# Kernel tuning notes

Measured on AMD Instinct MI355X. Metric: run time of the kernel, lower is better.

Reference implementation:

```python
import jax, jax.numpy as jnp
import numpy as np

B, F, V, K, D, H = 16384, 26, 100000, 16, 13, 400
IN_DIM = F * K + D  # 429
EPS = 1e-5


def _bn(x, g, b):
    # BatchNorm1d in training mode: batch statistics (biased var, like torch)
    m = jnp.mean(x, axis=0)
    v = jnp.mean((x - m) ** 2, axis=0)
    return g * (x - m) / jnp.sqrt(v + EPS) + b


def setup_inputs() -> dict:
    key = jax.random.key(0)
    ks = jax.random.split(key, 12)
    X_cat = jax.random.randint(ks[0], (B, F), 0, V)
    X_dense = jax.random.normal(ks[1], (B, D), dtype=jnp.float32)
    fm1_tables = jax.random.normal(ks[2], (F, V, 1), dtype=jnp.float32) * 0.01
    emb_tables = jax.random.normal(ks[3], (F, V, K), dtype=jnp.float32) * 0.01
    Wd = jax.random.normal(ks[4], (D, 1), dtype=jnp.float32) * 0.1
    bd = jnp.zeros((1,), jnp.float32)
    W1 = jax.random.normal(ks[5], (IN_DIM, H), dtype=jnp.float32) * (1.0 / np.sqrt(IN_DIM))
    b1 = jnp.zeros((H,), jnp.float32)
    g1 = jnp.ones((H,), jnp.float32)
    be1 = jnp.zeros((H,), jnp.float32)
    W2 = jax.random.normal(ks[6], (H, H), dtype=jnp.float32) * (1.0 / np.sqrt(H))
    b2 = jnp.zeros((H,), jnp.float32)
    g2 = jnp.ones((H,), jnp.float32)
    be2 = jnp.zeros((H,), jnp.float32)
    W3 = jax.random.normal(ks[7], (H, 1), dtype=jnp.float32) * (1.0 / np.sqrt(H))
    b3 = jnp.zeros((1,), jnp.float32)
    return dict(X_cat=X_cat, X_dense=X_dense, fm1_tables=fm1_tables,
                emb_tables=emb_tables, Wd=Wd, bd=bd, W1=W1, b1=b1, g1=g1,
                be1=be1, W2=W2, b2=b2, g2=g2, be2=be2, W3=W3, b3=b3)


def reference(X_cat, X_dense, fm1_tables, emb_tables, Wd, bd,
              W1, b1, g1, be1, W2, b2, g2, be2, W3, b3):
    gather = jax.vmap(lambda tab, idx: tab[idx], in_axes=(0, 1), out_axes=1)
    # 1st order: [B, F, 1] -> sum over fields -> [B, 1]
    y_1st = jnp.sum(gather(fm1_tables, X_cat), axis=1) + X_dense @ Wd + bd
    # 2nd order embeddings: [B, F, K]
    emb = gather(emb_tables, X_cat)
    s = jnp.sum(emb, axis=1)                 # [B, K]
    ix = s ** 2 - jnp.sum(emb ** 2, axis=1)  # [B, K]
    fm_y = 0.5 * jnp.sum(ix, axis=1, keepdims=True)
    # DNN on [flattened embeddings, dense]
    x = jnp.concatenate([emb.reshape(emb.shape[0], -1), X_dense], axis=1)
    h = jax.nn.relu(_bn(x @ W1 + b1, g1, be1))
    h = jax.nn.relu(_bn(h @ W2 + b2, g2, be2))
    dnn_y = h @ W3 + b3
    return y_1st + fm_y + dnn_y
```

## Files before the change

### kernel.cpp

```cpp
#include <hip/hip_runtime.h>
#include <stdint.h>

#define B_ROWS 16384
#define NF 26
#define NV 100000
#define ND 13
#define NH 400
#define XPAD 448
#define ZPAD 416
#define EPS 1e-5f

typedef __attribute__((ext_vector_type(8))) short short8;
typedef __attribute__((ext_vector_type(4))) float f32x4;
typedef __attribute__((ext_vector_type(4))) unsigned int uint4v;

__device__ inline float bf2f(unsigned short u) {
    union { unsigned int i; float f; } v; v.i = (unsigned int)u << 16; return v.f;
}
__device__ inline unsigned short f2bf(float f) {
    union { float f; unsigned int i; } v; v.f = f;
    return (unsigned short)((v.i + 0x7fff + ((v.i >> 16) & 1)) >> 16);
}

typedef __attribute__((address_space(1))) const unsigned int g_u32;
typedef __attribute__((address_space(3))) unsigned int l_u32;
__device__ __forceinline__ void gload_lds16(const void* g, void* l) {
    __builtin_amdgcn_global_load_lds((g_u32*)g, (l_u32*)l, 16, 0, 0);
}

#define X_OFF    0
#define Z1_OFF   14680064
#define W1S_OFF  28311552
#define W2S_OFF  28712960
#define BASE_OFF 29085696
#define ST_OFF   29151232

__global__ __launch_bounds__(256) void gather_prep(
    const int* __restrict__ Xcat, const float* __restrict__ Xdense,
    const float* __restrict__ fm1, const float* __restrict__ emb,
    const float* __restrict__ Wd, const float* __restrict__ bd,
    const float* __restrict__ W1, const float* __restrict__ W2,
    unsigned short* __restrict__ X, float* __restrict__ base,
    unsigned short* __restrict__ W1s, unsigned short* __restrict__ W2s,
    float* __restrict__ st)
{
    int tid = threadIdx.x;
    if (blockIdx.x >= 1024) {
        int c = (blockIdx.x - 1024) * 256 + tid;
        if (c < 256) {
            for (int i = tid; i < 6656; i += 256) st[i] = 0.f;
        }
        const float* W; unsigned short* dst; int K; int cc;
        if (c < 25088) { W = W1; dst = W1s; K = 429; cc = c; }
        else           { W = W2; dst = W2s; K = 400; cc = c - 25088; }
        int n  = cc % 448;
        int q  = (cc / 448) & 3;
        int kt = cc / 1792;
        unsigned short o[8];
        #pragma unroll
        for (int j = 0; j < 8; ++j) {
            int k = kt * 32 + q * 8 + j;
            float v = (n < NH && k < K) ? W[(size_t)k * NH + n] : 0.f;
            o[j] = f2bf(v);
        }
        *(uint4v*)(dst + (size_t)cc * 8) = *(uint4v*)o;
        return;
    }
    int r = blockIdx.x * 16 + (tid >> 4);
    int k = tid & 15;
    const int* idxp = Xcat + (size_t)r * NF;
    unsigned short* xrow = X + (size_t)r * XPAD;

    float s = 0.f, ss = 0.f;
    #pragma unroll
    for (int f = 0; f < NF; ++f) {
        int idx = idxp[f];
        float v = emb[((size_t)f * NV + idx) * 16 + k];
        s += v; ss += v * v;
        xrow[f * 16 + k] = f2bf(v);
    }
    float fmsum = fm1[(size_t)k * NV + idxp[k]];
    if (k < NF - 16) fmsum += fm1[(size_t)(k + 16) * NV + idxp[k + 16]];
    float dsum = 0.f;
    if (k < ND) {
        float xd = Xdense[(size_t)r * ND + k];
        dsum = xd * Wd[k];
        xrow[NF * 16 + k] = f2bf(xd);
    }
    xrow[429 + k] = 0;
    if (k < 3) xrow[445 + k] = 0;

    float ix = s * s - ss;
    float rf = fmsum, rd = dsum;
    #pragma unroll
    for (int off = 8; off; off >>= 1) {
        ix += __shfl_xor(ix, off, 16);
        rf += __shfl_xor(rf, off, 16);
        rd += __shfl_xor(rd, off, 16);
    }
    if (k == 0) base[r] = 0.5f * ix + rf + rd + bd[0];
}

template<int NT, int LDA, bool APPLY_BN>
__global__ __launch_bounds__(512, 2) void gemm_v2(
    const unsigned short* __restrict__ A,
    const unsigned short* __restrict__ Wst,
    const float* __restrict__ bias,
    const float* __restrict__ st_all,
    const float* __restrict__ g, const float* __restrict__ be,
    unsigned short* __restrict__ Z, int ldz, int padZ,
    float* __restrict__ st_out, int sumOff, int sqOff)
{
    __shared__ __align__(16) unsigned short slices[25600];
    __shared__ float alpha_s[416], beta_s[416];

    const int tid = threadIdx.x, bid = blockIdx.x;
    const int lane = tid & 63, wv = tid >> 6;
    const int rg = wv >> 2, w4 = wv & 3;
    const int l15 = lane & 15, qh = lane >> 4;
    const int cb = (w4 == 0) ? 0 : (112 + (w4 - 1) * 96);
    const int NFW = (w4 == 0) ? 7 : 6;
    unsigned short* slice =
        slices + rg * 12800 + ((w4 == 0) ? 0 : (3584 + (w4 - 1) * 3072));
    const int arowA = bid * 64 + rg * 32 + l15;
    const int arowB = arowA + 16;

    if constexpr (APPLY_BN) {
        for (int c = tid; c < ZPAD; c += 512) {
            float a = 0.f, b = 0.f;
            if (c < NH) {
                float gs = 0.f, gq = 0.f;
                #pragma unroll
                for (int cp = 0; cp < 4; ++cp) {
                    gs += st_all[cp * 1664 + c];
                    gq += st_all[cp * 1664 + 416 + c];
                }
                float mean = gs * (1.f / 16384.f);
                float var  = gq * (1.f / 16384.f) - mean * mean;
                a = g[c] * rsqrtf(var + EPS);
                b = be[c] - mean * a;
            }
            alpha_s[c] = a; beta_s[c] = b;
        }
        __syncthreads();
    }

    f32x4 acc0[7], acc1[7];
    #pragma unroll
    for (int i = 0; i < 7; ++i) { acc0[i] = f32x4{0,0,0,0}; acc1[i] = f32x4{0,0,0,0}; }

    auto stageW = [&](int kt) {
        #pragma unroll
        for (int i = 0; i < 7; ++i) if (i < NFW) {
            int ci = (kt * 4 + qh) * 448 + cb + i * 16 + l15;
            gload_lds16(Wst + (size_t)ci * 8, slice + i * 512);
        }
    };

    stageW(0);
    short8 afA_n = *(const short8*)(A + (size_t)arowA * LDA + qh * 8);
    short8 afB_n = *(const short8*)(A + (size_t)arowB * LDA + qh * 8);

    for (int kt = 0; kt < NT; ++kt) {
        asm volatile("s_waitcnt vmcnt(0)" ::: "memory");
        __builtin_amdgcn_sched_barrier(0);
        short8 bf[7];
        #pragma unroll
        for (int i = 0; i < 7; ++i) if (i < NFW)
            bf[i] = *(const short8*)(slice + i * 512 + lane * 8);
        short8 afA = afA_n, afB = afB_n;
        asm volatile("s_waitcnt lgkmcnt(0)" ::: "memory");
        __builtin_amdgcn_sched_barrier(0);
        if (kt + 1 < NT) {
            stageW(kt + 1);
            afA_n = *(const short8*)(A + (size_t)arowA * LDA + (kt + 1) * 32 + qh * 8);
            afB_n = *(const short8*)(A + (size_t)arowB * LDA + (kt + 1) * 32 + qh * 8);
        }
        if constexpr (APPLY_BN) {
            const int k0 = kt * 32 + qh * 8;
            #pragma unroll
            for (int j = 0; j < 8; ++j) {
                float fa = fmaxf(0.f, alpha_s[k0 + j] * bf2f((unsigned short)afA[j]) + beta_s[k0 + j]);
                float fb = fmaxf(0.f, alpha_s[k0 + j] * bf2f((unsigned short)afB[j]) + beta_s[k0 + j]);
                afA[j] = (short)f2bf(fa); afB[j] = (short)f2bf(fb);
            }
        }
        #pragma unroll
        for (int i = 0; i < 7; ++i) if (i < NFW) {
            acc0[i] = __builtin_amdgcn_mfma_f32_16x16x32_bf16(afA, bf[i], acc0[i], 0, 0, 0);
            acc1[i] = __builtin_amdgcn_mfma_f32_16x16x32_bf16(afB, bf[i], acc1[i], 0, 0, 0);
        }
    }

    float* stc = st_out + (bid & 3) * 1664;
    #pragma unroll
    for (int i = 0; i < 7; ++i) if (i < NFW) {
        int col = cb + i * 16 + l15;
        float bv = bias[col];
        float ps = 0.f, pq = 0.f;
        #pragma unroll
        for (int q = 0; q < 4; ++q) {
            float v0 = acc0[i][q] + bv;
            float v1 = acc1[i][q] + bv;
            Z[(size_t)(bid * 64 + rg * 32 + qh * 4 + q) * ldz + col] = f2bf(v0);
            Z[(size_t)(bid * 64 + rg * 32 + 16 + qh * 4 + q) * ldz + col] = f2bf(v1);
            ps += v0 + v1; pq += v0 * v0 + v1 * v1;
        }
        ps += __shfl_xor(ps, 16, 64); ps += __shfl_xor(ps, 32, 64);
        pq += __shfl_xor(pq, 16, 64); pq += __shfl_xor(pq, 32, 64);
        if (qh == 0) {
            atomicAdd(&stc[sumOff + col], ps);
            atomicAdd(&stc[sqOff + col], pq);
        }
    }
    if (padZ && w4 == 3) {
        #pragma unroll
        for (int rr = 0; rr < 8; ++rr)
            Z[(size_t)(bid * 64 + rg * 32 + rr * 4 + qh) * ldz + 400 + l15] = 0;
    }
}

__global__ __launch_bounds__(256) void final_kernel(
    const unsigned short* __restrict__ Z2,
    const float* __restrict__ st_all,
    const float* __restrict__ g2, const float* __restrict__ be2,
    const float* __restrict__ W3, const float* __restrict__ b3,
    const float* __restrict__ base, float* __restrict__ out)
{
    __shared__ float a2s[NH], b2s[NH], w3s[NH];
    int tid = threadIdx.x;
    for (int c = tid; c < NH; c += 256) {
        float gs = 0.f, gq = 0.f;
        #pragma unroll
        for (int cp = 0; cp < 4; ++cp) {
            gs += st_all[cp * 1664 + 832 + c];
            gq += st_all[cp * 1664 + 1248 + c];
        }
        float mean = gs * (1.f / 16384.f);
        float var  = gq * (1.f / 16384.f) - mean * mean;
        float a = g2[c] * rsqrtf(var + EPS);
        a2s[c] = a;
        b2s[c] = be2[c] - mean * a;
        w3s[c] = W3[c];
    }
    __syncthreads();
    int lane = tid & 63;
    int wv = tid >> 6;
    bool act = lane < 50;
    int cb = lane * 8;
    float al[8], bb[8], w3[8];
    #pragma unroll
    for (int j = 0; j < 8; ++j) {
        al[j] = act ? a2s[cb + j] : 0.f;
        bb[j] = act ? b2s[cb + j] : 0.f;
        w3[j] = act ? w3s[cb + j] : 0.f;
    }
    int r0 = blockIdx.x * 32 + wv * 8;
    float bias3 = b3[0];
    for (int t = 0; t < 8; t += 2) {
        int r = r0 + t;
        float acc0 = 0.f, acc1 = 0.f;
        if (act) {
            short8 z0 = *(const short8*)(Z2 + (size_t)r * ZPAD + cb);
            short8 z1 = *(const short8*)(Z2 + (size_t)(r + 1) * ZPAD + cb);
            #pragma unroll
            for (int j = 0; j < 8; ++j) {
                acc0 += fmaxf(0.f, al[j] * bf2f((unsigned short)z0[j]) + bb[j]) * w3[j];
                acc1 += fmaxf(0.f, al[j] * bf2f((unsigned short)z1[j]) + bb[j]) * w3[j];
            }
        }
        #pragma unroll
        for (int off = 32; off; off >>= 1) {
            acc0 += __shfl_xor(acc0, off, 64);
            acc1 += __shfl_xor(acc1, off, 64);
        }
        if (lane == 0) out[r] = base[r] + acc0 + bias3;
        if (lane == 1) out[r + 1] = base[r + 1] + acc1 + bias3;
    }
}

extern "C" void kernel_launch(void* const* d_in, const int* in_sizes, int n_in,
                              void* d_out, int out_size, void* d_ws, size_t ws_size,
                              hipStream_t stream)
{
    const int*   Xcat = (const int*)d_in[0];
    const float* Xd   = (const float*)d_in[1];
    const float* fm1  = (const float*)d_in[2];
    const float* emb  = (const float*)d_in[3];
    const float* Wd   = (const float*)d_in[4];
    const float* bd   = (const float*)d_in[5];
    const float* W1   = (const float*)d_in[6];
    const float* b1   = (const float*)d_in[7];
    const float* g1   = (const float*)d_in[8];
    const float* be1  = (const float*)d_in[9];
    const float* W2   = (const float*)d_in[10];
    const float* b2   = (const float*)d_in[11];
    const float* g2   = (const float*)d_in[12];
    const float* be2  = (const float*)d_in[13];
    const float* W3   = (const float*)d_in[14];
    const float* b3   = (const float*)d_in[15];

    char* ws = (char*)d_ws;
    unsigned short* X   = (unsigned short*)(ws + X_OFF);
    unsigned short* Z1  = (unsigned short*)(ws + Z1_OFF);
    unsigned short* Z2  = X;
    unsigned short* W1s = (unsigned short*)(ws + W1S_OFF);
    unsigned short* W2s = (unsigned short*)(ws + W2S_OFF);
    float* base = (float*)(ws + BASE_OFF);
    float* st   = (float*)(ws + ST_OFF);
    float* out  = (float*)d_out;

    gather_prep<<<1213, 256, 0, stream>>>(Xcat, Xd, fm1, emb, Wd, bd, W1, W2,
                                          X, base, W1s, W2s, st);

    gemm_v2<14, XPAD, false><<<256, 512, 0, stream>>>(
        X, W1s, b1, nullptr, nullptr, nullptr, Z1, ZPAD, 1, st, 0, 416);

    gemm_v2<13, ZPAD, true><<<256, 512, 0, stream>>>(
        Z1, W2s, b2, st, g1, be1, Z2, ZPAD, 0, st, 832, 1248);

    final_kernel<<<512, 256, 0, stream>>>(Z2, st, g2, be2, W3, b3, base, out);
}
```

Before: 73.48 us.

## Load GEMM weight fragments directly to registers and halve rows per block

The two MLP GEMM kernels no longer stage weight fragments through LDS with global_load_lds. Each wave now loads its B fragments straight from global memory into registers, double-buffered across k-steps. Each wave handles one 16-row tile instead of two, so blocks cover 32 rows, the grid doubles to 512, and launch bounds target higher occupancy. This removes LDS traffic and waits and spreads work over more CUs. The cost is that each weight fragment is reused by only one A tile, which doubles weight reads from global/L2.

```diff
diff --git a/kernel.cpp b/kernel.cpp
--- a/kernel.cpp
+++ b/kernel.cpp
@@ -20,12 +20,6 @@
 __device__ inline unsigned short f2bf(float f) {
     union { float f; unsigned int i; } v; v.f = f;
     return (unsigned short)((v.i + 0x7fff + ((v.i >> 16) & 1)) >> 16);
-}
-
-typedef __attribute__((address_space(1))) const unsigned int g_u32;
-typedef __attribute__((address_space(3))) unsigned int l_u32;
-__device__ __forceinline__ void gload_lds16(const void* g, void* l) {
-    __builtin_amdgcn_global_load_lds((g_u32*)g, (l_u32*)l, 16, 0, 0);
 }
 
 #define X_OFF    0
@@ -102,7 +96,7 @@
 }
 
 template<int NT, int LDA, bool APPLY_BN>
-__global__ __launch_bounds__(512, 2) void gemm_v2(
+__global__ __launch_bounds__(512, 4) void gemm_v3(
     const unsigned short* __restrict__ A,
     const unsigned short* __restrict__ Wst,
     const float* __restrict__ bias,
@@ -111,22 +105,19 @@
     unsigned short* __restrict__ Z, int ldz, int padZ,
     float* __restrict__ st_out, int sumOff, int sqOff)
 {
-    __shared__ __align__(16) unsigned short slices[25600];
     __shared__ float alpha_s[416], beta_s[416];
 
     const int tid = threadIdx.x, bid = blockIdx.x;
     const int lane = tid & 63, wv = tid >> 6;
-    const int rg = wv >> 2, w4 = wv & 3;
+    const int rh = wv >> 2, w4 = wv & 3;
     const int l15 = lane & 15, qh = lane >> 4;
     const int cb = (w4 == 0) ? 0 : (112 + (w4 - 1) * 96);
     const int NFW = (w4 == 0) ? 7 : 6;
-    unsigned short* slice =
-        slices + rg * 12800 + ((w4 == 0) ? 0 : (3584 + (w4 - 1) * 3072));
-    const int arowA = bid * 64 + rg * 32 + l15;
-    const int arowB = arowA + 16;
+    const int arow = bid * 32 + rh * 16 + l15;
 
     if constexpr (APPLY_BN) {
-        for (int c = tid; c < ZPAD; c += 512) {
+        if (tid < 416) {
+            int c = tid;
             float a = 0.f, b = 0.f;
             if (c < NH) {
                 float gs = 0.f, gq = 0.f;
@@ -145,51 +136,42 @@
         __syncthreads();
     }
 
-    f32x4 acc0[7], acc1[7];
-    #pragma unroll
-    for (int i = 0; i < 7; ++i) { acc0[i] = f32x4{0,0,0,0}; acc1[i] = f32x4{0,0,0,0}; }
-
-    auto stageW = [&](int kt) {
-        #pragma unroll
-        for (int i = 0; i < 7; ++i) if (i < NFW) {
-            int ci = (kt * 4 + qh) * 448 + cb + i * 16 + l15;
-            gload_lds16(Wst + (size_t)ci * 8, slice + i * 512);
-        }
+    f32x4 acc[7];
+    #pragma unroll
+    for (int i = 0; i < 7; ++i) acc[i] = f32x4{0.f, 0.f, 0.f, 0.f};
+
+    auto ldW = [&](int kt, short8* dst) {
+        #pragma unroll
+        for (int i = 0; i < 7; ++i) if (i < NFW)
+            dst[i] = *(const short8*)(
+                Wst + ((size_t)((kt * 4 + qh) * 448 + cb + i * 16 + l15)) * 8);
     };
 
-    stageW(0);
-    short8 afA_n = *(const short8*)(A + (size_t)arowA * LDA + qh * 8);
-    short8 afB_n = *(const short8*)(A + (size_t)arowB * LDA + qh * 8);
-
+    short8 bfn[7], afn;
+    ldW(0, bfn);
+    afn = *(const short8*)(A + (size_t)arow * LDA + qh * 8);
+
+    #pragma unroll 1
     for (int kt = 0; kt < NT; ++kt) {
-        asm volatile("s_waitcnt vmcnt(0)" ::: "memory");
-        __builtin_amdgcn_sched_barrier(0);
         short8 bf[7];
         #pragma unroll
-        for (int i = 0; i < 7; ++i) if (i < NFW)
-            bf[i] = *(const short8*)(slice + i * 512 + lane * 8);
-        short8 afA = afA_n, afB = afB_n;
-        asm volatile("s_waitcnt lgkmcnt(0)" ::: "memory");
-        __builtin_amdgcn_sched_barrier(0);
+        for (int i = 0; i < 7; ++i) bf[i] = bfn[i];
+        short8 af = afn;
         if (kt + 1 < NT) {
-            stageW(kt + 1);
-            afA_n = *(const short8*)(A + (size_t)arowA * LDA + (kt + 1) * 32 + qh * 8);
-            afB_n = *(const short8*)(A + (size_t)arowB * LDA + (kt + 1) * 32 + qh * 8);
+            ldW(kt + 1, bfn);
+            afn = *(const short8*)(A + (size_t)arow * LDA + (kt + 1) * 32 + qh * 8);
         }
         if constexpr (APPLY_BN) {
             const int k0 = kt * 32 + qh * 8;
             #pragma unroll
             for (int j = 0; j < 8; ++j) {
-                float fa = fmaxf(0.f, alpha_s[k0 + j] * bf2f((unsigned short)afA[j]) + beta_s[k0 + j]);
-                float fb = fmaxf(0.f, alpha_s[k0 + j] * bf2f((unsigned short)afB[j]) + beta_s[k0 + j]);
-                afA[j] = (short)f2bf(fa); afB[j] = (short)f2bf(fb);
+                float fa = fmaxf(0.f, alpha_s[k0 + j] * bf2f((unsigned short)af[j]) + beta_s[k0 + j]);
+                af[j] = (short)f2bf(fa);
             }
         }
         #pragma unroll
-        for (int i = 0; i < 7; ++i) if (i < NFW) {
-            acc0[i] = __builtin_amdgcn_mfma_f32_16x16x32_bf16(afA, bf[i], acc0[i], 0, 0, 0);
-            acc1[i] = __builtin_amdgcn_mfma_f32_16x16x32_bf16(afB, bf[i], acc1[i], 0, 0, 0);
-        }
+        for (int i = 0; i < 7; ++i) if (i < NFW)
+            acc[i] = __builtin_amdgcn_mfma_f32_16x16x32_bf16(af, bf[i], acc[i], 0, 0, 0);
     }
 
     float* stc = st_out + (bid & 3) * 1664;
@@ -200,11 +182,9 @@
         float ps = 0.f, pq = 0.f;
         #pragma unroll
         for (int q = 0; q < 4; ++q) {
-            float v0 = acc0[i][q] + bv;
-            float v1 = acc1[i][q] + bv;
-            Z[(size_t)(bid * 64 + rg * 32 + qh * 4 + q) * ldz + col] = f2bf(v0);
-            Z[(size_t)(bid * 64 + rg * 32 + 16 + qh * 4 + q) * ldz + col] = f2bf(v1);
-            ps += v0 + v1; pq += v0 * v0 + v1 * v1;
+            float v0 = acc[i][q] + bv;
+            Z[(size_t)(bid * 32 + rh * 16 + qh * 4 + q) * ldz + col] = f2bf(v0);
+            ps += v0; pq += v0 * v0;
         }
         ps += __shfl_xor(ps, 16, 64); ps += __shfl_xor(ps, 32, 64);
         pq += __shfl_xor(pq, 16, 64); pq += __shfl_xor(pq, 32, 64);
@@ -215,8 +195,8 @@
     }
     if (padZ && w4 == 3) {
         #pragma unroll
-        for (int rr = 0; rr < 8; ++rr)
-            Z[(size_t)(bid * 64 + rg * 32 + rr * 4 + qh) * ldz + 400 + l15] = 0;
+        for (int q = 0; q < 4; ++q)
+            Z[(size_t)(bid * 32 + rh * 16 + qh * 4 + q) * ldz + 400 + l15] = 0;
     }
 }
 
@@ -313,10 +293,10 @@
     gather_prep<<<1213, 256, 0, stream>>>(Xcat, Xd, fm1, emb, Wd, bd, W1, W2,
                                           X, base, W1s, W2s, st);
 
-    gemm_v2<14, XPAD, false><<<256, 512, 0, stream>>>(
+    gemm_v3<14, XPAD, false><<<512, 512, 0, stream>>>(
         X, W1s, b1, nullptr, nullptr, nullptr, Z1, ZPAD, 1, st, 0, 416);
 
-    gemm_v2<13, ZPAD, true><<<256, 512, 0, stream>>>(
+    gemm_v3<13, ZPAD, true><<<512, 512, 0, stream>>>(
         Z1, W2s, b2, st, g1, be1, Z2, ZPAD, 0, st, 832, 1248);
 
     final_kernel<<<512, 256, 0, stream>>>(Z2, st, g2, be2, W3, b3, base, out);
```

After: 240.4 us. 3.27x slower.

## Fuse both GEMMs and final reduction into one cooperative kernel with LDS-resident activations

Applied to the files above, without the earlier changes.

Replaces the two GEMM launches and the final kernel with one cooperative kernel. Each block keeps its 64-row Z1 and Z2 tiles in LDS instead of writing them to global memory and reading them back. Grid-wide syncs wait for the batch-norm statistics before each dependent stage. This removes two launches and the global round trips of the intermediate activations. In exchange it adds two grid barriers, and the roughly 112 KB of LDS per block limits the kernel to one block per CU.

```diff
diff --git a/kernel.cpp b/kernel.cpp
--- a/kernel.cpp
+++ b/kernel.cpp
@@ -1,5 +1,8 @@
 #include <hip/hip_runtime.h>
+#include <hip/hip_cooperative_groups.h>
 #include <stdint.h>
+
+namespace cg = cooperative_groups;
 
 #define B_ROWS 16384
 #define NF 26
@@ -8,6 +11,7 @@
 #define NH 400
 #define XPAD 448
 #define ZPAD 416
+#define Z1S  424
 #define EPS 1e-5f
 
 typedef __attribute__((ext_vector_type(8))) short short8;
@@ -29,11 +33,10 @@
 }
 
 #define X_OFF    0
-#define Z1_OFF   14680064
-#define W1S_OFF  28311552
-#define W2S_OFF  28712960
-#define BASE_OFF 29085696
-#define ST_OFF   29151232
+#define W1S_OFF  14680064
+#define W2S_OFF  15081472
+#define BASE_OFF 15454208
+#define ST_OFF   15519744
 
 __global__ __launch_bounds__(256) void gather_prep(
     const int* __restrict__ Xcat, const float* __restrict__ Xdense,
@@ -101,18 +104,25 @@
     if (k == 0) base[r] = 0.5f * ix + rf + rd + bd[0];
 }
 
-template<int NT, int LDA, bool APPLY_BN>
-__global__ __launch_bounds__(512, 2) void gemm_v2(
-    const unsigned short* __restrict__ A,
-    const unsigned short* __restrict__ Wst,
-    const float* __restrict__ bias,
-    const float* __restrict__ st_all,
-    const float* __restrict__ g, const float* __restrict__ be,
-    unsigned short* __restrict__ Z, int ldz, int padZ,
-    float* __restrict__ st_out, int sumOff, int sqOff)
+__global__ __launch_bounds__(512, 2) void deepfm_core(
+    const unsigned short* __restrict__ X,
+    const unsigned short* __restrict__ W1s,
+    const unsigned short* __restrict__ W2s,
+    const float* __restrict__ b1, const float* __restrict__ g1,
+    const float* __restrict__ be1,
+    const float* __restrict__ b2, const float* __restrict__ g2,
+    const float* __restrict__ be2,
+    const float* __restrict__ W3, const float* __restrict__ b3,
+    const float* __restrict__ base, float* __restrict__ st,
+    float* __restrict__ out)
 {
-    __shared__ __align__(16) unsigned short slices[25600];
-    __shared__ float alpha_s[416], beta_s[416];
+    cg::grid_group grid = cg::this_grid();
+    __shared__ __align__(16) char smem[114944];
+    unsigned short* slices = (unsigned short*)smem;
+    unsigned short* z1 = (unsigned short*)(smem + 57344);
+    float* alpha_s = (float*)(smem + 111616);
+    float* beta_s  = alpha_s + 416;
+    unsigned short* z2 = (unsigned short*)smem;
 
     const int tid = threadIdx.x, bid = blockIdx.x;
     const int lane = tid & 63, wv = tid >> 6;
@@ -120,36 +130,12 @@
     const int l15 = lane & 15, qh = lane >> 4;
     const int cb = (w4 == 0) ? 0 : (112 + (w4 - 1) * 96);
     const int NFW = (w4 == 0) ? 7 : 6;
-    unsigned short* slice =
-        slices + rg * 12800 + ((w4 == 0) ? 0 : (3584 + (w4 - 1) * 3072));
+    unsigned short* slice = slices + wv * 3584;
     const int arowA = bid * 64 + rg * 32 + l15;
     const int arowB = arowA + 16;
-
-    if constexpr (APPLY_BN) {
-        for (int c = tid; c < ZPAD; c += 512) {
-            float a = 0.f, b = 0.f;
-            if (c < NH) {
-                float gs = 0.f, gq = 0.f;
-                #pragma unroll
-                for (int cp = 0; cp < 4; ++cp) {
-                    gs += st_all[cp * 1664 + c];
-                    gq += st_all[cp * 1664 + 416 + c];
-                }
-                float mean = gs * (1.f / 16384.f);
-                float var  = gq * (1.f / 16384.f) - mean * mean;
-                a = g[c] * rsqrtf(var + EPS);
-                b = be[c] - mean * a;
-            }
-            alpha_s[c] = a; beta_s[c] = b;
-        }
-        __syncthreads();
-    }
-
-    f32x4 acc0[7], acc1[7];
-    #pragma unroll
-    for (int i = 0; i < 7; ++i) { acc0[i] = f32x4{0,0,0,0}; acc1[i] = f32x4{0,0,0,0}; }
-
-    auto stageW = [&](int kt) {
+    float* stc = st + (bid & 3) * 1664;
+
+    auto stageW = [&](const unsigned short* Wst, int kt) {
         #pragma unroll
         for (int i = 0; i < 7; ++i) if (i < NFW) {
             int ci = (kt * 4 + qh) * 448 + cb + i * 16 + l15;
@@ -157,11 +143,15 @@
         }
     };
 
-    stageW(0);
-    short8 afA_n = *(const short8*)(A + (size_t)arowA * LDA + qh * 8);
-    short8 afB_n = *(const short8*)(A + (size_t)arowB * LDA + qh * 8);
-
-    for (int kt = 0; kt < NT; ++kt) {
+    f32x4 acc0[7], acc1[7];
+    #pragma unroll
+    for (int i = 0; i < 7; ++i) { acc0[i] = f32x4{0,0,0,0}; acc1[i] = f32x4{0,0,0,0}; }
+
+    stageW(W1s, 0);
+    short8 afA_n = *(const short8*)(X + (size_t)arowA * XPAD + qh * 8);
+    short8 afB_n = *(const short8*)(X + (size_t)arowB * XPAD + qh * 8);
+
+    for (int kt = 0; kt < 14; ++kt) {
         asm volatile("s_waitcnt vmcnt(0)" ::: "memory");
         __builtin_amdgcn_sched_barrier(0);
         short8 bf[7];
@@ -171,19 +161,10 @@
         short8 afA = afA_n, afB = afB_n;
         asm volatile("s_waitcnt lgkmcnt(0)" ::: "memory");
         __builtin_amdgcn_sched_barrier(0);
-        if (kt + 1 < NT) {
-            stageW(kt + 1);
-            afA_n = *(const short8*)(A + (size_t)arowA * LDA + (kt + 1) * 32 + qh * 8);
-            afB_n = *(const short8*)(A + (size_t)arowB * LDA + (kt + 1) * 32 + qh * 8);
-        }
-        if constexpr (APPLY_BN) {
-            const int k0 = kt * 32 + qh * 8;
-            #pragma unroll
-            for (int j = 0; j < 8; ++j) {
-                float fa = fmaxf(0.f, alpha_s[k0 + j] * bf2f((unsigned short)afA[j]) + beta_s[k0 + j]);
-                float fb = fmaxf(0.f, alpha_s[k0 + j] * bf2f((unsigned short)afB[j]) + beta_s[k0 + j]);
-                afA[j] = (short)f2bf(fa); afB[j] = (short)f2bf(fb);
-            }
+        if (kt + 1 < 14) {
+            stageW(W1s, kt + 1);
+            afA_n = *(const short8*)(X + (size_t)arowA * XPAD + (kt + 1) * 32 + qh * 8);
+            afB_n = *(const short8*)(X + (size_t)arowB * XPAD + (kt + 1) * 32 + qh * 8);
         }
         #pragma unroll
         for (int i = 0; i < 7; ++i) if (i < NFW) {
@@ -192,90 +173,122 @@
         }
     }
 
-    float* stc = st_out + (bid & 3) * 1664;
     #pragma unroll
     for (int i = 0; i < 7; ++i) if (i < NFW) {
         int col = cb + i * 16 + l15;
-        float bv = bias[col];
+        float bv = b1[col];
         float ps = 0.f, pq = 0.f;
         #pragma unroll
         for (int q = 0; q < 4; ++q) {
             float v0 = acc0[i][q] + bv;
             float v1 = acc1[i][q] + bv;
-            Z[(size_t)(bid * 64 + rg * 32 + qh * 4 + q) * ldz + col] = f2bf(v0);
-            Z[(size_t)(bid * 64 + rg * 32 + 16 + qh * 4 + q) * ldz + col] = f2bf(v1);
+            z1[(size_t)(rg * 32 + qh * 4 + q) * Z1S + col] = f2bf(v0);
+            z1[(size_t)(rg * 32 + 16 + qh * 4 + q) * Z1S + col] = f2bf(v1);
             ps += v0 + v1; pq += v0 * v0 + v1 * v1;
         }
         ps += __shfl_xor(ps, 16, 64); ps += __shfl_xor(ps, 32, 64);
         pq += __shfl_xor(pq, 16, 64); pq += __shfl_xor(pq, 32, 64);
-        if (qh == 0) {
-            atomicAdd(&stc[sumOff + col], ps);
-            atomicAdd(&stc[sqOff + col], pq);
-        }
-    }
-    if (padZ && w4 == 3) {
+        if (qh == 0) { atomicAdd(&stc[col], ps); atomicAdd(&stc[416 + col], pq); }
+    }
+    if (w4 == 3) {
         #pragma unroll
         for (int rr = 0; rr < 8; ++rr)
-            Z[(size_t)(bid * 64 + rg * 32 + rr * 4 + qh) * ldz + 400 + l15] = 0;
-    }
-}
-
-__global__ __launch_bounds__(256) void final_kernel(
-    const unsigned short* __restrict__ Z2,
-    const float* __restrict__ st_all,
-    const float* __restrict__ g2, const float* __restrict__ be2,
-    const float* __restrict__ W3, const float* __restrict__ b3,
-    const float* __restrict__ base, float* __restrict__ out)
-{
-    __shared__ float a2s[NH], b2s[NH], w3s[NH];
-    int tid = threadIdx.x;
-    for (int c = tid; c < NH; c += 256) {
+            z1[(size_t)(rg * 32 + rr * 4 + qh) * Z1S + 400 + l15] = 0;
+    }
+    grid.sync();
+
+    for (int c = tid; c < ZPAD; c += 512) {
+        float a = 0.f, b = 0.f;
+        if (c < NH) {
+            float gs = 0.f, gq = 0.f;
+            #pragma unroll
+            for (int cp = 0; cp < 4; ++cp) {
+                gs += st[cp * 1664 + c];
+                gq += st[cp * 1664 + 416 + c];
+            }
+            float mean = gs * (1.f / 16384.f);
+            float var  = gq * (1.f / 16384.f) - mean * mean;
+            a = g1[c] * rsqrtf(var + EPS);
+            b = be1[c] - mean * a;
+        }
+        alpha_s[c] = a; beta_s[c] = b;
+    }
+    __syncthreads();
+
+    #pragma unroll
+    for (int i = 0; i < 7; ++i) { acc0[i] = f32x4{0,0,0,0}; acc1[i] = f32x4{0,0,0,0}; }
+    stageW(W2s, 0);
+
+    for (int kt = 0; kt < 13; ++kt) {
+        asm volatile("s_waitcnt vmcnt(0)" ::: "memory");
+        __builtin_amdgcn_sched_barrier(0);
+        short8 bf[7];
+        #pragma unroll
+        for (int i = 0; i < 7; ++i) if (i < NFW)
+            bf[i] = *(const short8*)(slice + i * 512 + lane * 8);
+        int k0 = kt * 32 + qh * 8;
+        short8 rA = *(const short8*)&z1[(size_t)(rg * 32 + l15) * Z1S + k0];
+        short8 rB = *(const short8*)&z1[(size_t)(rg * 32 + 16 + l15) * Z1S + k0];
+        asm volatile("s_waitcnt lgkmcnt(0)" ::: "memory");
+        __builtin_amdgcn_sched_barrier(0);
+        if (kt + 1 < 13) stageW(W2s, kt + 1);
+        short8 afA, afB;
+        #pragma unroll
+        for (int j = 0; j < 8; ++j) {
+            float al = alpha_s[k0 + j], bt = beta_s[k0 + j];
+            afA[j] = (short)f2bf(fmaxf(0.f, al * bf2f((unsigned short)rA[j]) + bt));
+            afB[j] = (short)f2bf(fmaxf(0.f, al * bf2f((unsigned short)rB[j]) + bt));
+        }
+        #pragma unroll
+        for (int i = 0; i < 7; ++i) if (i < NFW) {
+            acc0[i] = __builtin_amdgcn_mfma_f32_16x16x32_bf16(afA, bf[i], acc0[i], 0, 0, 0);
+            acc1[i] = __builtin_amdgcn_mfma_f32_16x16x32_bf16(afB, bf[i], acc1[i], 0, 0, 0);
+        }
+    }
+
+    __syncthreads();
+    #pragma unroll
+    for (int i = 0; i < 7; ++i) if (i < NFW) {
+        int col = cb + i * 16 + l15;
+        float bv = b2[col];
+        float ps = 0.f, pq = 0.f;
+        #pragma unroll
+        for (int q = 0; q < 4; ++q) {
+            float v0 = acc0[i][q] + bv;
+            float v1 = acc1[i][q] + bv;
+            z2[(size_t)(rg * 32 + qh * 4 + q) * 400 + col] = f2bf(v0);
+            z2[(size_t)(rg * 32 + 16 + qh * 4 + q) * 400 + col] = f2bf(v1);
+            ps += v0 + v1; pq += v0 * v0 + v1 * v1;
+        }
+        ps += __shfl_xor(ps, 16, 64); ps += __shfl_xor(ps, 32, 64);
+        pq += __shfl_xor(pq, 16, 64); pq += __shfl_xor(pq, 32, 64);
+        if (qh == 0) { atomicAdd(&stc[832 + col], ps); atomicAdd(&stc[1248 + col], pq); }
+    }
+    grid.sync();
+
+    for (int c = tid; c < NH; c += 512) {
         float gs = 0.f, gq = 0.f;
         #pragma unroll
         for (int cp = 0; cp < 4; ++cp) {
-            gs += st_all[cp * 1664 + 832 + c];
-            gq += st_all[cp * 1664 + 1248 + c];
+            gs += st[cp * 1664 + 832 + c];
+            gq += st[cp * 1664 + 1248 + c];
         }
         float mean = gs * (1.f / 16384.f);
         float var  = gq * (1.f / 16384.f) - mean * mean;
         float a = g2[c] * rsqrtf(var + EPS);
-        a2s[c] = a;
-        b2s[c] = be2[c] - mean * a;
-        w3s[c] = W3[c];
+        alpha_s[c] = a;
+        beta_s[c]  = be2[c] - mean * a;
     }
     __syncthreads();
-    int lane = tid & 63;
-    int wv = tid >> 6;
-    bool act = lane < 50;
-    int cb = lane * 8;
-    float al[8], bb[8], w3[8];
-    #pragma unroll
-    for (int j = 0; j < 8; ++j) {
-        al[j] = act ? a2s[cb + j] : 0.f;
-        bb[j] = act ? b2s[cb + j] : 0.f;
-        w3[j] = act ? w3s[cb + j] : 0.f;
-    }
-    int r0 = blockIdx.x * 32 + wv * 8;
-    float bias3 = b3[0];
-    for (int t = 0; t < 8; t += 2) {
-        int r = r0 + t;
-        float acc0 = 0.f, acc1 = 0.f;
-        if (act) {
-            short8 z0 = *(const short8*)(Z2 + (size_t)r * ZPAD + cb);
-            short8 z1 = *(const short8*)(Z2 + (size_t)(r + 1) * ZPAD + cb);
-            #pragma unroll
-            for (int j = 0; j < 8; ++j) {
-                acc0 += fmaxf(0.f, al[j] * bf2f((unsigned short)z0[j]) + bb[j]) * w3[j];
-                acc1 += fmaxf(0.f, al[j] * bf2f((unsigned short)z1[j]) + bb[j]) * w3[j];
-            }
-        }
-        #pragma unroll
-        for (int off = 32; off; off >>= 1) {
-            acc0 += __shfl_xor(acc0, off, 64);
-            acc1 += __shfl_xor(acc1, off, 64);
-        }
-        if (lane == 0) out[r] = base[r] + acc0 + bias3;
-        if (lane == 1) out[r + 1] = base[r + 1] + acc1 + bias3;
+    {
+        int r = tid >> 3, oct = tid & 7;
+        float facc = 0.f;
+        for (int c = oct; c < NH; c += 8)
+            facc += fmaxf(0.f, alpha_s[c] * bf2f(z2[(size_t)r * 400 + c]) + beta_s[c]) * W3[c];
+        facc += __shfl_xor(facc, 1, 64);
+        facc += __shfl_xor(facc, 2, 64);
+        facc += __shfl_xor(facc, 4, 64);
+        if (oct == 0) out[bid * 64 + r] = base[bid * 64 + r] + facc + b3[0];
     }
 }
 
@@ -302,8 +315,6 @@
 
     char* ws = (char*)d_ws;
     unsigned short* X   = (unsigned short*)(ws + X_OFF);
-    unsigned short* Z1  = (unsigned short*)(ws + Z1_OFF);
-    unsigned short* Z2  = X;
     unsigned short* W1s = (unsigned short*)(ws + W1S_OFF);
     unsigned short* W2s = (unsigned short*)(ws + W2S_OFF);
     float* base = (float*)(ws + BASE_OFF);
@@ -313,11 +324,13 @@
     gather_prep<<<1213, 256, 0, stream>>>(Xcat, Xd, fm1, emb, Wd, bd, W1, W2,
                                           X, base, W1s, W2s, st);
 
-    gemm_v2<14, XPAD, false><<<256, 512, 0, stream>>>(
-        X, W1s, b1, nullptr, nullptr, nullptr, Z1, ZPAD, 1, st, 0, 416);
-
-    gemm_v2<13, ZPAD, true><<<256, 512, 0, stream>>>(
-        Z1, W2s, b2, st, g1, be1, Z2, ZPAD, 0, st, 832, 1248);
-
-    final_kernel<<<512, 256, 0, stream>>>(Z2, st, g2, be2, W3, b3, base, out);
-}
+    void* args[] = {
+        (void*)&X, (void*)&W1s, (void*)&W2s,
+        (void*)&b1, (void*)&g1, (void*)&be1,
+        (void*)&b2, (void*)&g2, (void*)&be2,
+        (void*)&W3, (void*)&b3,
+        (void*)&base, (void*)&st, (void*)&out
+    };
+    hipLaunchCooperativeKernel((const void*)deepfm_core, dim3(256), dim3(512),
+                               args, 0, stream);
+}
```

Result: slower. 130.8 us (+78.0%).

## Double-buffer weight slices in GEMM kernels with two-stage prefetch

Applied to the files above, without the earlier changes.

Doubles the LDS weight staging buffer and restructures the K loop into ping-pong phases that prefetch tile kt+2 while computing kt. Partial vmcnt waits let the next stage's loads stay in flight instead of draining all memory ops each iteration. This hides more global/async-LDS latency behind MFMA work. The cost is twice the shared memory (about 100KB per block), which may limit occupancy at two blocks per CU, plus extra live A-fragment registers.

```diff
diff --git a/kernel.cpp b/kernel.cpp
--- a/kernel.cpp
+++ b/kernel.cpp
@@ -102,7 +102,7 @@
 }
 
 template<int NT, int LDA, bool APPLY_BN>
-__global__ __launch_bounds__(512, 2) void gemm_v2(
+__global__ __launch_bounds__(512, 2) void gemm_v5(
     const unsigned short* __restrict__ A,
     const unsigned short* __restrict__ Wst,
     const float* __restrict__ bias,
@@ -111,7 +111,7 @@
     unsigned short* __restrict__ Z, int ldz, int padZ,
     float* __restrict__ st_out, int sumOff, int sqOff)
 {
-    __shared__ __align__(16) unsigned short slices[25600];
+    __shared__ __align__(16) unsigned short slices[51200];
     __shared__ float alpha_s[416], beta_s[416];
 
     const int tid = threadIdx.x, bid = blockIdx.x;
@@ -120,13 +120,13 @@
     const int l15 = lane & 15, qh = lane >> 4;
     const int cb = (w4 == 0) ? 0 : (112 + (w4 - 1) * 96);
     const int NFW = (w4 == 0) ? 7 : 6;
-    unsigned short* slice =
-        slices + rg * 12800 + ((w4 == 0) ? 0 : (3584 + (w4 - 1) * 3072));
+    const int soff = rg * 12800 + ((w4 == 0) ? 0 : (3584 + (w4 - 1) * 3072));
     const int arowA = bid * 64 + rg * 32 + l15;
     const int arowB = arowA + 16;
 
     if constexpr (APPLY_BN) {
-        for (int c = tid; c < ZPAD; c += 512) {
+        if (tid < 416) {
+            int c = tid;
             float a = 0.f, b = 0.f;
             if (c < NH) {
                 float gs = 0.f, gq = 0.f;
@@ -149,47 +149,75 @@
     #pragma unroll
     for (int i = 0; i < 7; ++i) { acc0[i] = f32x4{0,0,0,0}; acc1[i] = f32x4{0,0,0,0}; }
 
-    auto stageW = [&](int kt) {
+    auto stageW = [&](int kt, int buf) {
+        unsigned short* sl = slices + buf * 25600 + soff;
         #pragma unroll
         for (int i = 0; i < 7; ++i) if (i < NFW) {
             int ci = (kt * 4 + qh) * 448 + cb + i * 16 + l15;
-            gload_lds16(Wst + (size_t)ci * 8, slice + i * 512);
-        }
-    };
-
-    stageW(0);
-    short8 afA_n = *(const short8*)(A + (size_t)arowA * LDA + qh * 8);
-    short8 afB_n = *(const short8*)(A + (size_t)arowB * LDA + qh * 8);
-
-    for (int kt = 0; kt < NT; ++kt) {
+            gload_lds16(Wst + (size_t)ci * 8, sl + i * 512);
+        }
+    };
+    auto ldA = [&](int kt, short8& a, short8& b) {
+        a = *(const short8*)(A + (size_t)arowA * LDA + kt * 32 + qh * 8);
+        b = *(const short8*)(A + (size_t)arowB * LDA + kt * 32 + qh * 8);
+    };
+    auto waitN = [&]() {
+        if (w4 == 0) asm volatile("s_waitcnt vmcnt(9)" ::: "memory");
+        else         asm volatile("s_waitcnt vmcnt(8)" ::: "memory");
+        __builtin_amdgcn_sched_barrier(0);
+    };
+    auto wait0 = [&]() {
         asm volatile("s_waitcnt vmcnt(0)" ::: "memory");
         __builtin_amdgcn_sched_barrier(0);
-        short8 bf[7];
-        #pragma unroll
-        for (int i = 0; i < 7; ++i) if (i < NFW)
-            bf[i] = *(const short8*)(slice + i * 512 + lane * 8);
-        short8 afA = afA_n, afB = afB_n;
+    };
+    auto waitlg = [&]() {
         asm volatile("s_waitcnt lgkmcnt(0)" ::: "memory");
         __builtin_amdgcn_sched_barrier(0);
-        if (kt + 1 < NT) {
-            stageW(kt + 1);
-            afA_n = *(const short8*)(A + (size_t)arowA * LDA + (kt + 1) * 32 + qh * 8);
-            afB_n = *(const short8*)(A + (size_t)arowB * LDA + (kt + 1) * 32 + qh * 8);
-        }
+    };
+
+    auto phase = [&](int kt, int buf, bool last, bool issue,
+                     short8& afA, short8& afB) {
+        if (last) wait0(); else waitN();
+        const unsigned short* sl = slices + buf * 25600 + soff;
+        short8 bf[7];
+        #pragma unroll
+        for (int i = 0; i < 7; ++i) if (i < NFW)
+            bf[i] = *(const short8*)(sl + i * 512 + lane * 8);
+        short8 aA = afA, aB = afB;
+        waitlg();
+        if (issue) { stageW(kt + 2, buf); ldA(kt + 2, afA, afB); }
         if constexpr (APPLY_BN) {
             const int k0 = kt * 32 + qh * 8;
             #pragma unroll
             for (int j = 0; j < 8; ++j) {
-                float fa = fmaxf(0.f, alpha_s[k0 + j] * bf2f((unsigned short)afA[j]) + beta_s[k0 + j]);
-                float fb = fmaxf(0.f, alpha_s[k0 + j] * bf2f((unsigned short)afB[j]) + beta_s[k0 + j]);
-                afA[j] = (short)f2bf(fa); afB[j] = (short)f2bf(fb);
+                float al = alpha_s[k0 + j], bt = beta_s[k0 + j];
+                aA[j] = (short)f2bf(fmaxf(0.f, al * bf2f((unsigned short)aA[j]) + bt));
+                aB[j] = (short)f2bf(fmaxf(0.f, al * bf2f((unsigned short)aB[j]) + bt));
             }
         }
         #pragma unroll
         for (int i = 0; i < 7; ++i) if (i < NFW) {
-            acc0[i] = __builtin_amdgcn_mfma_f32_16x16x32_bf16(afA, bf[i], acc0[i], 0, 0, 0);
-            acc1[i] = __builtin_amdgcn_mfma_f32_16x16x32_bf16(afB, bf[i], acc1[i], 0, 0, 0);
-        }
+            acc0[i] = __builtin_amdgcn_mfma_f32_16x16x32_bf16(aA, bf[i], acc0[i], 0, 0, 0);
+            acc1[i] = __builtin_amdgcn_mfma_f32_16x16x32_bf16(aB, bf[i], acc1[i], 0, 0, 0);
+        }
+    };
+
+    short8 afA0, afB0, afA1, afB1;
+    stageW(0, 0); ldA(0, afA0, afB0);
+    stageW(1, 1); ldA(1, afA1, afB1);
+
+    int kt2 = 0;
+    for (; kt2 + 3 < NT; kt2 += 2) {
+        phase(kt2,     0, false, true, afA0, afB0);
+        phase(kt2 + 1, 1, false, true, afA1, afB1);
+    }
+    if constexpr (NT % 2 == 0) {
+        phase(NT - 2, 0, false, false, afA0, afB0);
+        phase(NT - 1, 1, true,  false, afA1, afB1);
+    } else {
+        phase(NT - 3, 0, false, true,  afA0, afB0);
+        phase(NT - 2, 1, false, false, afA1, afB1);
+        phase(NT - 1, 0, true,  false, afA0, afB0);
     }
 
     float* stc = st_out + (bid & 3) * 1664;
@@ -313,10 +341,10 @@
     gather_prep<<<1213, 256, 0, stream>>>(Xcat, Xd, fm1, emb, Wd, bd, W1, W2,
                                           X, base, W1s, W2s, st);
 
-    gemm_v2<14, XPAD, false><<<256, 512, 0, stream>>>(
+    gemm_v5<14, XPAD, false><<<256, 512, 0, stream>>>(
         X, W1s, b1, nullptr, nullptr, nullptr, Z1, ZPAD, 1, st, 0, 416);
 
-    gemm_v2<13, ZPAD, true><<<256, 512, 0, stream>>>(
+    gemm_v5<13, ZPAD, true><<<256, 512, 0, stream>>>(
         Z1, W2s, b2, st, g1, be1, Z2, ZPAD, 0, st, 832, 1248);
 
     final_kernel<<<512, 256, 0, stream>>>(Z2, st, g2, be2, W3, b3, base, out);
```

New measurement: 72.64 us (median of 2 runs). No clear change (-1.1%).
